# Optimization experiments

Hardware: AMD Instinct MI355X
Metric: run time of the kernel (lower is better)

The kernel has to match this reference:

```python
import jax, jax.numpy as jnp
import numpy as np

B, NPG, H, D = 16, 4096, 2, 64            # graphs, nodes/graph, heads, in_channels
N = B * NPG                                # 65536 total nodes
E_PER = 32768                              # edges per graph (avg degree 8)
E = B * E_PER                              # 524288 total edges
K_ORDER = 4
BETA = 0.5
D_OUT = 64


def setup_inputs():
    key = jax.random.key(0)
    k = jax.random.split(key, 10)
    x = jax.random.normal(k[0], (N, D), jnp.float32)
    # intra-graph random edges (block-diagonal adjacency)
    src = jax.random.randint(k[1], (B, E_PER), 0, NPG)
    dst = jax.random.randint(k[2], (B, E_PER), 0, NPG)
    off = (jnp.arange(B) * NPG)[:, None]
    edge_index = jnp.stack([(src + off).reshape(-1), (dst + off).reshape(-1)], axis=0)
    batch = jnp.arange(N) // NPG
    s = 1.0 / np.sqrt(D)
    Wq = jax.random.normal(k[3], (D, D * H), jnp.float32) * s
    bq = jnp.zeros((D * H,), jnp.float32)
    Wk = jax.random.normal(k[4], (D, D * H), jnp.float32) * s
    bk = jnp.zeros((D * H,), jnp.float32)
    Wo = jax.random.normal(k[5], (D * H, D_OUT), jnp.float32) * (1.0 / np.sqrt(D * H))
    bo = jnp.zeros((D_OUT,), jnp.float32)
    return {"x": x, "edge_index": edge_index, "batch": batch,
            "Wq": Wq, "bq": bq, "Wk": Wk, "bk": bk, "Wo": Wo, "bo": bo}


def reference(x, edge_index, batch, Wq, bq, Wk, bk, Wo, bo):
    Nn = x.shape[0]
    q = (x @ Wq + bq).reshape(Nn, H, D)
    k = (x @ Wk + bk).reshape(Nn, H, D)
    qs = q / jnp.linalg.norm(q, axis=2, keepdims=True)
    ks = k / jnp.linalg.norm(k, axis=2, keepdims=True)

    # symmetric-normalized transposed adjacency: adj_t[col_e, row_e] = w_e
    row, col = edge_index[0], edge_index[1]
    w = jnp.ones((row.shape[0],), x.dtype)
    deg = jax.ops.segment_sum(w, col, num_segments=N)
    dinv = jnp.where(deg > 0, deg ** -0.5, 0.0)
    val = dinv[col] * w * dinv[row]

    def gcn(xs):  # xs [N,H,D]; out[i] = sum_{e: col_e==i} val_e * xs[row_e]
        return jax.ops.segment_sum(val[:, None, None] * xs[row], col, num_segments=N)

    # ragged block <-> padded batch conversion (block-sorted batch ids)
    counts = jax.ops.segment_sum(jnp.ones((Nn,), jnp.int32), batch, num_segments=B)
    starts = jnp.concatenate([jnp.zeros((1,), jnp.int32), jnp.cumsum(counts)[:-1]])
    pos = jnp.arange(Nn) - starts[batch]

    def to_batch(v):
        return jnp.zeros((B, NPG) + v.shape[1:], v.dtype).at[batch, pos].set(v)

    def to_block(v):
        return v[batch, pos]

    qs_b, ks_b = to_batch(qs), to_batch(ks)      # [B, NPG, H, D]
    xs = jnp.broadcast_to(x[:, None, :], (Nn, H, D))
    xs_b = to_batch(xs)

    # linear (kernelized) attention; note source adds B (=qs.shape[0]) to the
    # denominator and uses the pre-loop xs_batch for every iteration -- kept faithful.
    kvs = jnp.einsum('blhm,blhd->bhmd', ks_b, xs_b)
    qkvs = jnp.einsum('bnhm,bhmd->bnhd', qs_b, kvs)
    num = qkvs + xs_b.sum(axis=1)[:, None]                       # [B,NPG,H,D]
    den = jnp.einsum('bnhm,bhm->bnh', qs_b, ks_b.sum(axis=1))[..., None] + float(B)
    attn_blk = to_block(num / den)                               # [N,H,D]

    for _ in range(K_ORDER):
        xs = xs + BETA * gcn(xs) + (1.0 - BETA) * attn_blk

    return (xs.reshape(Nn, H * D) @ Wo + bo) / H
```

## Files before the change

kernel.cpp:

```cpp
#include <hip/hip_runtime.h>

#define N_NODES 65536
#define B_G     16
#define NPG_    4096
#define H_H     2
#define D_D     64
#define HD      128
#define E_E     524288
#define D_OUT   64


__global__ void deg_kernel(const int* __restrict__ col, int* __restrict__ degi) {
    int e = blockIdx.x * 256 + threadIdx.x;
    if (e < E_E) atomicAdd(&degi[col[e]], 1);
}

__global__ void scan1(const int* __restrict__ degi, int* __restrict__ ptr,
                      int* __restrict__ bsums, float* __restrict__ dinv) {
    __shared__ int lds[256];
    int t = threadIdx.x;
    int i = blockIdx.x * 256 + t;
    int v = degi[i];
    dinv[i] = (v > 0) ? (1.0f / sqrtf((float)v)) : 0.0f;
    lds[t] = v;
    __syncthreads();
    for (int off = 1; off < 256; off <<= 1) {
        int tmp = (t >= off) ? lds[t - off] : 0;
        __syncthreads();
        lds[t] += tmp;
        __syncthreads();
    }
    ptr[i] = lds[t] - v;
    if (t == 255) bsums[blockIdx.x] = lds[255];
}

__global__ void scan3(int* __restrict__ ptr, const int* __restrict__ bsums) {
    __shared__ int red[256];
    int t = threadIdx.x;
    red[t] = (t < (int)blockIdx.x) ? bsums[t] : 0;
    __syncthreads();
    for (int off = 128; off > 0; off >>= 1) {
        if (t < off) red[t] += red[t + off];
        __syncthreads();
    }
    int i = blockIdx.x * 256 + t;
    ptr[i] += red[0];
    if (i == 0) ptr[N_NODES] = E_E;
}

__global__ void scatter_kernel(const int* __restrict__ row, const int* __restrict__ col,
                               const int* __restrict__ ptr, int* __restrict__ cursor,
                               const float* __restrict__ dinv,
                               int2* __restrict__ ep) {
    int e = blockIdx.x * 256 + threadIdx.x;
    if (e < E_E) {
        int c = col[e], r = row[e];
        int p = ptr[c] + atomicAdd(&cursor[c], 1);
        ep[p] = make_int2(r, __float_as_int(dinv[c] * dinv[r]));
    }
}

__global__ __launch_bounds__(256) void proj_kernel(
    const float* __restrict__ x,
    const float* __restrict__ Wq, const float* __restrict__ bq,
    const float* __restrict__ Wk, const float* __restrict__ bk,
    float* __restrict__ qs, float* __restrict__ ks) {
    __shared__ float4 wt4[16 * 64];
    __shared__ float4 xt4[128 * 16];
    int t = threadIdx.x;
    int qk = blockIdx.x & 1;
    int hh = (blockIdx.x >> 1) & 1;
    int nb = (blockIdx.x >> 2) * 128;
    const float* W = qk ? Wk : Wq;
    const float* bias = qk ? bk : bq;
    float* outp = qk ? ks : qs;

    for (int i = t; i < 1024; i += 256) {
        int k4 = i >> 6, c = i & 63;
        int cc = hh * 64 + c;
        wt4[i] = make_float4(W[(4 * k4 + 0) * 128 + cc], W[(4 * k4 + 1) * 128 + cc],
                             W[(4 * k4 + 2) * 128 + cc], W[(4 * k4 + 3) * 128 + cc]);
    }
    const float4* xg = (const float4*)(x + (size_t)nb * 64);
    for (int i = t; i < 2048; i += 256) {
        int node = i >> 4, k4 = i & 15;
        xt4[node * 16 + (k4 ^ (node & 7))] = xg[i];
    }
    __syncthreads();

    int cg = t & 15;
    int ns = t >> 4;
    int sw = ns & 7;

    float acc[8][4];
#pragma unroll
    for (int i = 0; i < 8; ++i)
#pragma unroll
        for (int j = 0; j < 4; ++j) acc[i][j] = 0.f;

    for (int k4 = 0; k4 < 16; ++k4) {
        float4 wv[4];
#pragma unroll
        for (int j = 0; j < 4; ++j) wv[j] = wt4[k4 * 64 + cg + 16 * j];
        int kx = k4 ^ sw;
#pragma unroll
        for (int i = 0; i < 8; ++i) {
            float4 xv = xt4[(ns + 16 * i) * 16 + kx];
#pragma unroll
            for (int j = 0; j < 4; ++j)
                acc[i][j] += wv[j].x * xv.x + wv[j].y * xv.y +
                             wv[j].z * xv.z + wv[j].w * xv.w;
        }
    }

    float bcol[4];
#pragma unroll
    for (int j = 0; j < 4; ++j) bcol[j] = bias[hh * 64 + cg + 16 * j];

#pragma unroll
    for (int i = 0; i < 8; ++i) {
#pragma unroll
        for (int j = 0; j < 4; ++j) acc[i][j] += bcol[j];
        float s = acc[i][0] * acc[i][0] + acc[i][1] * acc[i][1] +
                  acc[i][2] * acc[i][2] + acc[i][3] * acc[i][3];
#pragma unroll
        for (int off = 8; off > 0; off >>= 1) s += __shfl_xor(s, off);
        float r = rsqrtf(s);
        size_t base = (size_t)(nb + ns + 16 * i) * 128 + hh * 64 + cg;
#pragma unroll
        for (int j = 0; j < 4; ++j) outp[base + 16 * j] = acc[i][j] * r;
    }
}

__global__ __launch_bounds__(256) void kvs_part(
    const float* __restrict__ ks, const float* __restrict__ x,
    float* __restrict__ partials, float* __restrict__ ksum, float* __restrict__ xsum) {
    int bid = blockIdx.x;
    int chunk = bid & 31;
    int bh = bid >> 5;
    int b = bh >> 1, h = bh & 1;
    int t = threadIdx.x;
    int mrow = t >> 4, dcol = t & 15;
    int m0 = mrow * 4, d0 = dcol * 4;
    __shared__ float kl[32 * 64];
    __shared__ float xl[32 * 64];
    float acc[4][4] = {{0}};
    float ksacc[4] = {0, 0, 0, 0};
    float xsacc[4] = {0, 0, 0, 0};
    int node0 = b * NPG_ + chunk * 128;
    for (int s = 0; s < 4; ++s) {
        int nb = node0 + s * 32;
        for (int i = t; i < 512; i += 256) {
            int l = i >> 4, q = i & 15;
            ((float4*)kl)[i] = *(const float4*)(ks + (size_t)(nb + l) * 128 + h * 64 + q * 4);
        }
        const float4* xg = (const float4*)(x + (size_t)nb * 64);
        for (int i = t; i < 512; i += 256) ((float4*)xl)[i] = xg[i];
        __syncthreads();
        for (int l = 0; l < 32; ++l) {
            float4 kv = *(float4*)(kl + l * 64 + m0);
            float4 xv = *(float4*)(xl + l * 64 + d0);
            float kk[4] = {kv.x, kv.y, kv.z, kv.w};
            float xx[4] = {xv.x, xv.y, xv.z, xv.w};
#pragma unroll
            for (int i = 0; i < 4; ++i)
#pragma unroll
                for (int j = 0; j < 4; ++j) acc[i][j] += kk[i] * xx[j];
            if (dcol == 0) {
#pragma unroll
                for (int i = 0; i < 4; ++i) ksacc[i] += kk[i];
            }
            if (mrow == 0) {
#pragma unroll
                for (int j = 0; j < 4; ++j) xsacc[j] += xx[j];
            }
        }
        __syncthreads();
    }
    float* pout = partials + (size_t)bid * 4096;
#pragma unroll
    for (int i = 0; i < 4; ++i)
        *(float4*)(pout + (m0 + i) * 64 + d0) =
            make_float4(acc[i][0], acc[i][1], acc[i][2], acc[i][3]);
    if (dcol == 0) {
#pragma unroll
        for (int i = 0; i < 4; ++i) atomicAdd(&ksum[bh * 64 + m0 + i], ksacc[i]);
    }
    if (mrow == 0 && h == 0) {
#pragma unroll
        for (int j = 0; j < 4; ++j) atomicAdd(&xsum[b * 64 + d0 + j], xsacc[j]);
    }
}

__global__ __launch_bounds__(256) void kvs_reduce(
    const float* __restrict__ partials, float* __restrict__ kvs) {
    int i = blockIdx.x * 256 + threadIdx.x;
    int bh = i >> 12, elem = i & 4095;
    const float* p = partials + (size_t)bh * 32 * 4096 + elem;
    float s = 0.f;
#pragma unroll
    for (int c = 0; c < 32; ++c) s += p[c * 4096];
    kvs[i] = s;
}

__global__ __launch_bounds__(256) void mwo_kernel(
    const float* __restrict__ kvs, const float* __restrict__ Wo,
    const float* __restrict__ xsum, float* __restrict__ M, float* __restrict__ C) {
    __shared__ float kv_l[64 * 64];
    __shared__ float wo_l[64 * 64];
    __shared__ float xs_l[64];
    int bh = blockIdx.x;
    int b = bh >> 1, h = bh & 1;
    int t = threadIdx.x;
    const float4* kvg = (const float4*)(kvs + (size_t)bh * 4096);
    for (int i = t; i < 1024; i += 256) ((float4*)kv_l)[i] = kvg[i];
    for (int i = t; i < 1024; i += 256) {
        int d = i >> 4;
        ((float4*)wo_l)[i] = *(const float4*)(Wo + (size_t)(h * 64 + d) * 64 + (i & 15) * 4);
    }
    if (t < 64) xs_l[t] = xsum[b * 64 + t];
    __syncthreads();

    int ccol = t & 15, mrow = t >> 4;
    int m0 = mrow * 4, c0 = ccol * 4;
    float acc[4][4] = {{0.f}};
    float cacc[4] = {0.f, 0.f, 0.f, 0.f};
    for (int d = 0; d < 64; ++d) {
        float4 wv = *(const float4*)(wo_l + d * 64 + c0);
        float kvv[4];
#pragma unroll
        for (int i = 0; i < 4; ++i) kvv[i] = kv_l[(m0 + i) * 64 + d];
#pragma unroll
        for (int i = 0; i < 4; ++i) {
            acc[i][0] += kvv[i] * wv.x; acc[i][1] += kvv[i] * wv.y;
            acc[i][2] += kvv[i] * wv.z; acc[i][3] += kvv[i] * wv.w;
        }
        if (mrow == 0) {
            float xv = xs_l[d];
            cacc[0] += xv * wv.x; cacc[1] += xv * wv.y;
            cacc[2] += xv * wv.z; cacc[3] += xv * wv.w;
        }
    }
    float* mo = M + (size_t)bh * 4096;
#pragma unroll
    for (int i = 0; i < 4; ++i)
        *(float4*)(mo + (m0 + i) * 64 + c0) =
            make_float4(acc[i][0], acc[i][1], acc[i][2], acc[i][3]);
    if (mrow == 0)
        *(float4*)(C + bh * 64 + c0) = make_float4(cacc[0], cacc[1], cacc[2], cacc[3]);
}

__global__ __launch_bounds__(256) void fatt_kernel(
    const float* __restrict__ qs, const float* __restrict__ M,
    const float* __restrict__ C, const float* __restrict__ ksum,
    float* __restrict__ a) {
    __shared__ float4 wt4[16 * 64];
    __shared__ float4 xt4[64 * 16];
    __shared__ float4 ksv[16];
    __shared__ float csv[64];
    int nb = blockIdx.x * 64;
    int b = nb >> 12;
    int t = threadIdx.x;
    int cg = t & 15;
    int ns = t >> 4;
    int sw = ns & 3;
    int n_t = ns * 4;

    float acc[4][4] = {{0.f}};

    for (int h = 0; h < 2; ++h) {
        int bh = b * 2 + h;
        const float* mp = M + (size_t)bh * 4096;
        for (int i = t; i < 1024; i += 256) {
            int k4 = i >> 6, c = i & 63;
            wt4[i] = make_float4(mp[(4 * k4 + 0) * 64 + c], mp[(4 * k4 + 1) * 64 + c],
                                 mp[(4 * k4 + 2) * 64 + c], mp[(4 * k4 + 3) * 64 + c]);
        }
        for (int i = t; i < 1024; i += 256) {
            int node = i >> 4, k4 = i & 15;
            xt4[i] = *(const float4*)(qs + (size_t)(nb + node) * 128 + h * 64 + 4 * k4);
        }
        if (t < 16) ksv[t] = *(const float4*)(ksum + bh * 64 + 4 * t);
        if (t < 64) csv[t] = C[bh * 64 + t];
        __syncthreads();

        float pacc[4][4] = {{0.f}};
        float den[4] = {0.f, 0.f, 0.f, 0.f};
        for (int k4 = 0; k4 < 16; ++k4) {
            int kk = k4 ^ sw;
            float4 kv = ksv[kk];
            float4 wv[4];
#pragma unroll
            for (int j = 0; j < 4; ++j) wv[j] = wt4[kk * 64 + cg + 16 * j];
#pragma unroll
            for (int i = 0; i < 4; ++i) {
                float4 xv = xt4[(n_t + i) * 16 + kk];
                den[i] += kv.x * xv.x + kv.y * xv.y + kv.z * xv.z + kv.w * xv.w;
#pragma unroll
                for (int j = 0; j < 4; ++j)
                    pacc[i][j] += wv[j].x * xv.x + wv[j].y * xv.y +
                                  wv[j].z * xv.z + wv[j].w * xv.w;
            }
        }
        float cc[4];
#pragma unroll
        for (int j = 0; j < 4; ++j) cc[j] = csv[cg + 16 * j];
#pragma unroll
        for (int i = 0; i < 4; ++i) {
            float inv = 1.0f / (den[i] + 16.0f);
#pragma unroll
            for (int j = 0; j < 4; ++j) acc[i][j] += (pacc[i][j] + cc[j]) * inv;
        }
        __syncthreads();
    }

#pragma unroll
    for (int i = 0; i < 4; ++i)
#pragma unroll
        for (int j = 0; j < 4; ++j)
            a[(size_t)(nb + n_t + i) * 64 + cg + 16 * j] = acc[i][j];
}

__global__ __launch_bounds__(256) void y0_kernel(
    const float* __restrict__ x, const float* __restrict__ Wo,
    float* __restrict__ y0) {
    __shared__ float4 wt4[16 * 64];
    __shared__ float4 xt4[64 * 16];
    int t = threadIdx.x;
    int nb = blockIdx.x * 64;

    for (int i = t; i < 1024; i += 256) {
        int k4 = i >> 6, c = i & 63;
        wt4[i] = make_float4(
            Wo[(4 * k4 + 0) * 64 + c] + Wo[(4 * k4 + 64) * 64 + c],
            Wo[(4 * k4 + 1) * 64 + c] + Wo[(4 * k4 + 65) * 64 + c],
            Wo[(4 * k4 + 2) * 64 + c] + Wo[(4 * k4 + 66) * 64 + c],
            Wo[(4 * k4 + 3) * 64 + c] + Wo[(4 * k4 + 67) * 64 + c]);
    }
    const float4* xg = (const float4*)(x + (size_t)nb * 64);
    for (int i = t; i < 1024; i += 256) xt4[i] = xg[i];
    __syncthreads();

    int cg = t & 15;
    int ns = t >> 4;
    int s = ns & 3;
    int n_t = ns * 4;

    float acc[4][4] = {{0.f}};
#pragma unroll 4
    for (int k4 = 0; k4 < 16; ++k4) {
        int kk = k4 ^ s;
        float4 xv0 = xt4[(n_t + 0) * 16 + kk];
        float4 xv1 = xt4[(n_t + 1) * 16 + kk];
        float4 xv2 = xt4[(n_t + 2) * 16 + kk];
        float4 xv3 = xt4[(n_t + 3) * 16 + kk];
#pragma unroll
        for (int j = 0; j < 4; ++j) {
            float4 wv = wt4[kk * 64 + cg + 16 * j];
            acc[0][j] += wv.x * xv0.x + wv.y * xv0.y + wv.z * xv0.z + wv.w * xv0.w;
            acc[1][j] += wv.x * xv1.x + wv.y * xv1.y + wv.z * xv1.z + wv.w * xv1.w;
            acc[2][j] += wv.x * xv2.x + wv.y * xv2.y + wv.z * xv2.z + wv.w * xv2.w;
            acc[3][j] += wv.x * xv3.x + wv.y * xv3.y + wv.z * xv3.z + wv.w * xv3.w;
        }
    }
#pragma unroll
    for (int i = 0; i < 4; ++i)
#pragma unroll
        for (int j = 0; j < 4; ++j)
            y0[(size_t)(nb + n_t + i) * 64 + cg + 16 * j] = acc[i][j];
}

template <int LAST>
__global__ __launch_bounds__(256) void gcn64_kernel(
    const float* __restrict__ yin, const float* __restrict__ a,
    const int* __restrict__ ptr, const int2* __restrict__ ep,
    float* __restrict__ yout, const float* __restrict__ bo) {
    int bid = blockIdx.x;
    int lbid = (bid & 7) * (N_NODES / 16 / 8) + (bid >> 3);
    int t = threadIdx.x;
    int n = lbid * 16 + (t >> 4);
    int lg = t & 15;
    int c4 = lg * 4;
    int e0 = ptr[n], e1 = ptr[n + 1];
    int cnt = e1 - e0;
    float4 acc = make_float4(0.f, 0.f, 0.f, 0.f);

    int2 q[16];
#pragma unroll
    for (int i = 0; i < 16; ++i) {
        int ee = e0 + i;
        if (ee > e1 - 1) ee = e1 - 1;
        if (ee < 0) ee = 0;
        q[i] = ep[ee];
    }
#pragma unroll
    for (int i = 0; i < 16; ++i) {
        if (i < cnt) {
            float v = __int_as_float(q[i].y);
            float4 xv = *(const float4*)(yin + (size_t)q[i].x * 64 + c4);
            acc.x += v * xv.x; acc.y += v * xv.y;
            acc.z += v * xv.z; acc.w += v * xv.w;
        }
    }
    for (int e = e0 + 16; e < e1; ++e) {
        int2 qq = ep[e];
        float v = __int_as_float(qq.y);
        float4 xv = *(const float4*)(yin + (size_t)qq.x * 64 + c4);
        acc.x += v * xv.x; acc.y += v * xv.y;
        acc.z += v * xv.z; acc.w += v * xv.w;
    }

    size_t idx = (size_t)n * 64 + c4;
    float4 self = *(const float4*)(yin + idx);
    float4 at = *(const float4*)(a + idx);
    float4 o;
    o.x = self.x + 0.5f * acc.x + 0.5f * at.x;
    o.y = self.y + 0.5f * acc.y + 0.5f * at.y;
    o.z = self.z + 0.5f * acc.z + 0.5f * at.z;
    o.w = self.w + 0.5f * acc.w + 0.5f * at.w;
    if (LAST) {
        float4 bv = *(const float4*)(bo + c4);
        o.x = (o.x + bv.x) * 0.5f;
        o.y = (o.y + bv.y) * 0.5f;
        o.z = (o.z + bv.z) * 0.5f;
        o.w = (o.w + bv.w) * 0.5f;
    }
    *(float4*)(yout + idx) = o;
}


extern "C" void kernel_launch(void* const* d_in, const int* in_sizes, int n_in,
                              void* d_out, int out_size, void* d_ws, size_t ws_size,
                              hipStream_t stream) {
    const float* x  = (const float*)d_in[0];
    const int* ei   = (const int*)d_in[1];
    const float* Wq = (const float*)d_in[3];
    const float* bq = (const float*)d_in[4];
    const float* Wk = (const float*)d_in[5];
    const float* bk = (const float*)d_in[6];
    const float* Wo = (const float*)d_in[7];
    const float* bo = (const float*)d_in[8];
    float* out = (float*)d_out;

    const int* row = ei;
    const int* col = ei + E_E;

    float* bufA = (float*)d_ws;
    float* bufB = bufA + (size_t)N_NODES * HD;
    float* bufC = bufB + (size_t)N_NODES * HD;
    int2*  ep   = (int2*)(bufC + (size_t)N_NODES * HD);
    float* kvs  = (float*)(ep + E_E);
    float* M    = kvs + 131072;
    float* Cc   = M + 131072;
    float* ksum = Cc + 2048;
    float* xsum = ksum + 2048;
    float* dinv = xsum + 1024;
    int* degi   = (int*)(dinv + N_NODES);
    int* cursor = degi + N_NODES;
    int* ptr    = cursor + N_NODES;
    int* bsums  = ptr + N_NODES + 1;

    float* qs_      = bufC;
    float* ks_      = bufB;
    float* a_       = bufA;
    float* yA       = bufA + (size_t)N_NODES * 64;
    float* partials = yA;
    float* yB       = bufB;

    hipMemsetAsync(degi, 0, (size_t)N_NODES * 2 * 4, stream);
    hipMemsetAsync(ksum, 0, (size_t)(2048 + 1024) * 4, stream);

    deg_kernel<<<E_E / 256, 256, 0, stream>>>(col, degi);
    scan1<<<N_NODES / 256, 256, 0, stream>>>(degi, ptr, bsums, dinv);
    scan3<<<N_NODES / 256, 256, 0, stream>>>(ptr, bsums);
    scatter_kernel<<<E_E / 256, 256, 0, stream>>>(row, col, ptr, cursor, dinv, ep);

    proj_kernel<<<2048, 256, 0, stream>>>(x, Wq, bq, Wk, bk, qs_, ks_);

    kvs_part<<<1024, 256, 0, stream>>>(ks_, x, partials, ksum, xsum);
    kvs_reduce<<<512, 256, 0, stream>>>(partials, kvs);
    mwo_kernel<<<32, 256, 0, stream>>>(kvs, Wo, xsum, M, Cc);
    fatt_kernel<<<1024, 256, 0, stream>>>(qs_, M, Cc, ksum, a_);

    y0_kernel<<<1024, 256, 0, stream>>>(x, Wo, yA);

    gcn64_kernel<0><<<N_NODES / 16, 256, 0, stream>>>(yA, a_, ptr, ep, yB, bo);
    gcn64_kernel<0><<<N_NODES / 16, 256, 0, stream>>>(yB, a_, ptr, ep, yA, bo);
    gcn64_kernel<0><<<N_NODES / 16, 256, 0, stream>>>(yA, a_, ptr, ep, yB, bo);
    gcn64_kernel<1><<<N_NODES / 16, 256, 0, stream>>>(yB, a_, ptr, ep, out, bo);
}
```

Baseline: 336.3 us.

## Fuse q/k projections into KV-reduction and attention kernels, drop qs/ks buffers

Removes the standalone projection kernel. The K projection and normalization now run inside the KV partial-sum kernel, which uses 64-node chunks and produces twice as many partials. The Q projection runs inside the attention kernel per head. This avoids writing and re-reading two N×128 float intermediates in global memory. In exchange, each block reloads the Wq/Wk tiles, uses more shared memory, and adds a sync. The reduce kernel now sums 64 partials instead of 32.

```diff
diff --git a/kernel.cpp b/kernel.cpp
--- a/kernel.cpp
+++ b/kernel.cpp
@@ -60,133 +60,103 @@
     }
 }
 
-__global__ __launch_bounds__(256) void proj_kernel(
+__global__ __launch_bounds__(256) void kvskp_kernel(
     const float* __restrict__ x,
-    const float* __restrict__ Wq, const float* __restrict__ bq,
     const float* __restrict__ Wk, const float* __restrict__ bk,
-    float* __restrict__ qs, float* __restrict__ ks) {
+    float* __restrict__ partials, float* __restrict__ ksum, float* __restrict__ xsum) {
+    __shared__ float4 xt4[64 * 16];
     __shared__ float4 wt4[16 * 64];
-    __shared__ float4 xt4[128 * 16];
-    int t = threadIdx.x;
-    int qk = blockIdx.x & 1;
-    int hh = (blockIdx.x >> 1) & 1;
-    int nb = (blockIdx.x >> 2) * 128;
-    const float* W = qk ? Wk : Wq;
-    const float* bias = qk ? bk : bq;
-    float* outp = qk ? ks : qs;
-
+    __shared__ float4 kt4[64 * 16];
+    int bid = blockIdx.x;
+    int chunk = bid & 63;
+    int bh = bid >> 6;
+    int b = bh >> 1, h = bh & 1;
+    int node0 = b * NPG_ + chunk * 64;
+    int t = threadIdx.x;
+
+    const float4* xg = (const float4*)(x + (size_t)node0 * 64);
+    for (int i = t; i < 1024; i += 256) xt4[i] = xg[i];
     for (int i = t; i < 1024; i += 256) {
         int k4 = i >> 6, c = i & 63;
-        int cc = hh * 64 + c;
-        wt4[i] = make_float4(W[(4 * k4 + 0) * 128 + cc], W[(4 * k4 + 1) * 128 + cc],
-                             W[(4 * k4 + 2) * 128 + cc], W[(4 * k4 + 3) * 128 + cc]);
-    }
-    const float4* xg = (const float4*)(x + (size_t)nb * 64);
-    for (int i = t; i < 2048; i += 256) {
-        int node = i >> 4, k4 = i & 15;
-        xt4[node * 16 + (k4 ^ (node & 7))] = xg[i];
+        int cc = h * 64 + c;
+        wt4[i] = make_float4(Wk[(4 * k4 + 0) * 128 + cc], Wk[(4 * k4 + 1) * 128 + cc],
+                             Wk[(4 * k4 + 2) * 128 + cc], Wk[(4 * k4 + 3) * 128 + cc]);
     }
     __syncthreads();
 
     int cg = t & 15;
     int ns = t >> 4;
-    int sw = ns & 7;
-
-    float acc[8][4];
-#pragma unroll
-    for (int i = 0; i < 8; ++i)
-#pragma unroll
-        for (int j = 0; j < 4; ++j) acc[i][j] = 0.f;
-
-    for (int k4 = 0; k4 < 16; ++k4) {
-        float4 wv[4];
-#pragma unroll
-        for (int j = 0; j < 4; ++j) wv[j] = wt4[k4 * 64 + cg + 16 * j];
-        int kx = k4 ^ sw;
-#pragma unroll
-        for (int i = 0; i < 8; ++i) {
-            float4 xv = xt4[(ns + 16 * i) * 16 + kx];
+    int s = ns & 3;
+    int n_t = ns * 4;
+    float* ktf = (float*)kt4;
+
+    {
+        float acc[4][4] = {{0.f}};
+        for (int k4 = 0; k4 < 16; ++k4) {
+            int kk = k4 ^ s;
+            float4 wv[4];
+#pragma unroll
+            for (int j = 0; j < 4; ++j) wv[j] = wt4[kk * 64 + cg + 16 * j];
+#pragma unroll
+            for (int i = 0; i < 4; ++i) {
+                float4 xv = xt4[(n_t + i) * 16 + kk];
+#pragma unroll
+                for (int j = 0; j < 4; ++j)
+                    acc[i][j] += wv[j].x * xv.x + wv[j].y * xv.y +
+                                 wv[j].z * xv.z + wv[j].w * xv.w;
+            }
+        }
+        float bcol[4];
+#pragma unroll
+        for (int j = 0; j < 4; ++j) bcol[j] = bk[h * 64 + cg + 16 * j];
+#pragma unroll
+        for (int i = 0; i < 4; ++i) {
+#pragma unroll
+            for (int j = 0; j < 4; ++j) acc[i][j] += bcol[j];
+            float sq = acc[i][0] * acc[i][0] + acc[i][1] * acc[i][1] +
+                       acc[i][2] * acc[i][2] + acc[i][3] * acc[i][3];
+#pragma unroll
+            for (int off = 8; off > 0; off >>= 1) sq += __shfl_xor(sq, off);
+            float r = rsqrtf(sq);
 #pragma unroll
             for (int j = 0; j < 4; ++j)
-                acc[i][j] += wv[j].x * xv.x + wv[j].y * xv.y +
-                             wv[j].z * xv.z + wv[j].w * xv.w;
-        }
-    }
-
-    float bcol[4];
-#pragma unroll
-    for (int j = 0; j < 4; ++j) bcol[j] = bias[hh * 64 + cg + 16 * j];
-
-#pragma unroll
-    for (int i = 0; i < 8; ++i) {
-#pragma unroll
-        for (int j = 0; j < 4; ++j) acc[i][j] += bcol[j];
-        float s = acc[i][0] * acc[i][0] + acc[i][1] * acc[i][1] +
-                  acc[i][2] * acc[i][2] + acc[i][3] * acc[i][3];
-#pragma unroll
-        for (int off = 8; off > 0; off >>= 1) s += __shfl_xor(s, off);
-        float r = rsqrtf(s);
-        size_t base = (size_t)(nb + ns + 16 * i) * 128 + hh * 64 + cg;
-#pragma unroll
-        for (int j = 0; j < 4; ++j) outp[base + 16 * j] = acc[i][j] * r;
-    }
-}
-
-__global__ __launch_bounds__(256) void kvs_part(
-    const float* __restrict__ ks, const float* __restrict__ x,
-    float* __restrict__ partials, float* __restrict__ ksum, float* __restrict__ xsum) {
-    int bid = blockIdx.x;
-    int chunk = bid & 31;
-    int bh = bid >> 5;
-    int b = bh >> 1, h = bh & 1;
-    int t = threadIdx.x;
-    int mrow = t >> 4, dcol = t & 15;
-    int m0 = mrow * 4, d0 = dcol * 4;
-    __shared__ float kl[32 * 64];
-    __shared__ float xl[32 * 64];
-    float acc[4][4] = {{0}};
-    float ksacc[4] = {0, 0, 0, 0};
-    float xsacc[4] = {0, 0, 0, 0};
-    int node0 = b * NPG_ + chunk * 128;
-    for (int s = 0; s < 4; ++s) {
-        int nb = node0 + s * 32;
-        for (int i = t; i < 512; i += 256) {
-            int l = i >> 4, q = i & 15;
-            ((float4*)kl)[i] = *(const float4*)(ks + (size_t)(nb + l) * 128 + h * 64 + q * 4);
-        }
-        const float4* xg = (const float4*)(x + (size_t)nb * 64);
-        for (int i = t; i < 512; i += 256) ((float4*)xl)[i] = xg[i];
-        __syncthreads();
-        for (int l = 0; l < 32; ++l) {
-            float4 kv = *(float4*)(kl + l * 64 + m0);
-            float4 xv = *(float4*)(xl + l * 64 + d0);
-            float kk[4] = {kv.x, kv.y, kv.z, kv.w};
-            float xx[4] = {xv.x, xv.y, xv.z, xv.w};
-#pragma unroll
-            for (int i = 0; i < 4; ++i)
-#pragma unroll
-                for (int j = 0; j < 4; ++j) acc[i][j] += kk[i] * xx[j];
-            if (dcol == 0) {
-#pragma unroll
-                for (int i = 0; i < 4; ++i) ksacc[i] += kk[i];
-            }
-            if (mrow == 0) {
-#pragma unroll
-                for (int j = 0; j < 4; ++j) xsacc[j] += xx[j];
-            }
-        }
-        __syncthreads();
+                ktf[(n_t + i) * 64 + cg + 16 * j] = acc[i][j] * r;
+        }
+    }
+    __syncthreads();
+
+    int m0 = ns * 4, d0 = cg * 4;
+    float acc[4][4] = {{0.f}};
+    float ksacc[4] = {0.f, 0.f, 0.f, 0.f};
+    float xsacc[4] = {0.f, 0.f, 0.f, 0.f};
+    for (int l = 0; l < 64; ++l) {
+        float4 kv = *(const float4*)(ktf + l * 64 + m0);
+        float4 xv = xt4[l * 16 + cg];
+        float kk[4] = {kv.x, kv.y, kv.z, kv.w};
+        float xx[4] = {xv.x, xv.y, xv.z, xv.w};
+#pragma unroll
+        for (int i = 0; i < 4; ++i)
+#pragma unroll
+            for (int j = 0; j < 4; ++j) acc[i][j] += kk[i] * xx[j];
+        if (cg == 0) {
+#pragma unroll
+            for (int i = 0; i < 4; ++i) ksacc[i] += kk[i];
+        }
+        if (ns == 0) {
+#pragma unroll
+            for (int j = 0; j < 4; ++j) xsacc[j] += xx[j];
+        }
     }
     float* pout = partials + (size_t)bid * 4096;
 #pragma unroll
     for (int i = 0; i < 4; ++i)
         *(float4*)(pout + (m0 + i) * 64 + d0) =
             make_float4(acc[i][0], acc[i][1], acc[i][2], acc[i][3]);
-    if (dcol == 0) {
+    if (cg == 0) {
 #pragma unroll
         for (int i = 0; i < 4; ++i) atomicAdd(&ksum[bh * 64 + m0 + i], ksacc[i]);
     }
-    if (mrow == 0 && h == 0) {
+    if (ns == 0 && h == 0) {
 #pragma unroll
         for (int j = 0; j < 4; ++j) atomicAdd(&xsum[b * 64 + d0 + j], xsacc[j]);
     }
@@ -196,10 +166,10 @@
     const float* __restrict__ partials, float* __restrict__ kvs) {
     int i = blockIdx.x * 256 + threadIdx.x;
     int bh = i >> 12, elem = i & 4095;
-    const float* p = partials + (size_t)bh * 32 * 4096 + elem;
+    const float* p = partials + (size_t)bh * 64 * 4096 + elem;
     float s = 0.f;
 #pragma unroll
-    for (int c = 0; c < 32; ++c) s += p[c * 4096];
+    for (int c = 0; c < 64; ++c) s += p[c * 4096];
     kvs[i] = s;
 }
 
@@ -251,11 +221,13 @@
 }
 
 __global__ __launch_bounds__(256) void fatt_kernel(
-    const float* __restrict__ qs, const float* __restrict__ M,
-    const float* __restrict__ C, const float* __restrict__ ksum,
-    float* __restrict__ a) {
-    __shared__ float4 wt4[16 * 64];
+    const float* __restrict__ x,
+    const float* __restrict__ Wq, const float* __restrict__ bq,
+    const float* __restrict__ M, const float* __restrict__ C,
+    const float* __restrict__ ksum, float* __restrict__ a) {
     __shared__ float4 xt4[64 * 16];
+    __shared__ float4 wu4[16 * 64];
+    __shared__ float4 qt4[64 * 16];
     __shared__ float4 ksv[16];
     __shared__ float csv[64];
     int nb = blockIdx.x * 64;
@@ -265,20 +237,62 @@
     int ns = t >> 4;
     int sw = ns & 3;
     int n_t = ns * 4;
+    float* qtf = (float*)qt4;
+
+    const float4* xg = (const float4*)(x + (size_t)nb * 64);
+    for (int i = t; i < 1024; i += 256) xt4[i] = xg[i];
 
     float acc[4][4] = {{0.f}};
 
     for (int h = 0; h < 2; ++h) {
         int bh = b * 2 + h;
+        __syncthreads();
+        for (int i = t; i < 1024; i += 256) {
+            int k4 = i >> 6, c = i & 63;
+            int cc = h * 64 + c;
+            wu4[i] = make_float4(Wq[(4 * k4 + 0) * 128 + cc], Wq[(4 * k4 + 1) * 128 + cc],
+                                 Wq[(4 * k4 + 2) * 128 + cc], Wq[(4 * k4 + 3) * 128 + cc]);
+        }
+        __syncthreads();
+        {
+            float qa[4][4] = {{0.f}};
+            for (int k4 = 0; k4 < 16; ++k4) {
+                int kk = k4 ^ sw;
+                float4 wv[4];
+#pragma unroll
+                for (int j = 0; j < 4; ++j) wv[j] = wu4[kk * 64 + cg + 16 * j];
+#pragma unroll
+                for (int i = 0; i < 4; ++i) {
+                    float4 xv = xt4[(n_t + i) * 16 + kk];
+#pragma unroll
+                    for (int j = 0; j < 4; ++j)
+                        qa[i][j] += wv[j].x * xv.x + wv[j].y * xv.y +
+                                    wv[j].z * xv.z + wv[j].w * xv.w;
+                }
+            }
+            float bcol[4];
+#pragma unroll
+            for (int j = 0; j < 4; ++j) bcol[j] = bq[h * 64 + cg + 16 * j];
+#pragma unroll
+            for (int i = 0; i < 4; ++i) {
+#pragma unroll
+                for (int j = 0; j < 4; ++j) qa[i][j] += bcol[j];
+                float sq = qa[i][0] * qa[i][0] + qa[i][1] * qa[i][1] +
+                           qa[i][2] * qa[i][2] + qa[i][3] * qa[i][3];
+#pragma unroll
+                for (int off = 8; off > 0; off >>= 1) sq += __shfl_xor(sq, off);
+                float r = rsqrtf(sq);
+#pragma unroll
+                for (int j = 0; j < 4; ++j)
+                    qtf[(n_t + i) * 64 + cg + 16 * j] = qa[i][j] * r;
+            }
+        }
+        __syncthreads();
         const float* mp = M + (size_t)bh * 4096;
         for (int i = t; i < 1024; i += 256) {
             int k4 = i >> 6, c = i & 63;
-            wt4[i] = make_float4(mp[(4 * k4 + 0) * 64 + c], mp[(4 * k4 + 1) * 64 + c],
+            wu4[i] = make_float4(mp[(4 * k4 + 0) * 64 + c], mp[(4 * k4 + 1) * 64 + c],
                                  mp[(4 * k4 + 2) * 64 + c], mp[(4 * k4 + 3) * 64 + c]);
-        }
-        for (int i = t; i < 1024; i += 256) {
-            int node = i >> 4, k4 = i & 15;
-            xt4[i] = *(const float4*)(qs + (size_t)(nb + node) * 128 + h * 64 + 4 * k4);
         }
         if (t < 16) ksv[t] = *(const float4*)(ksum + bh * 64 + 4 * t);
         if (t < 64) csv[t] = C[bh * 64 + t];
@@ -291,10 +305,10 @@
             float4 kv = ksv[kk];
             float4 wv[4];
 #pragma unroll
-            for (int j = 0; j < 4; ++j) wv[j] = wt4[kk * 64 + cg + 16 * j];
+            for (int j = 0; j < 4; ++j) wv[j] = wu4[kk * 64 + cg + 16 * j];
 #pragma unroll
             for (int i = 0; i < 4; ++i) {
-                float4 xv = xt4[(n_t + i) * 16 + kk];
+                float4 xv = qt4[(n_t + i) * 16 + kk];
                 den[i] += kv.x * xv.x + kv.y * xv.y + kv.z * xv.z + kv.w * xv.w;
 #pragma unroll
                 for (int j = 0; j < 4; ++j)
@@ -311,7 +325,6 @@
 #pragma unroll
             for (int j = 0; j < 4; ++j) acc[i][j] += (pacc[i][j] + cc[j]) * inv;
         }
-        __syncthreads();
     }
 
 #pragma unroll
@@ -460,12 +473,10 @@
     int* ptr    = cursor + N_NODES;
     int* bsums  = ptr + N_NODES + 1;
 
-    float* qs_      = bufC;
-    float* ks_      = bufB;
     float* a_       = bufA;
     float* yA       = bufA + (size_t)N_NODES * 64;
-    float* partials = yA;
     float* yB       = bufB;
+    float* partials = bufC;
 
     hipMemsetAsync(degi, 0, (size_t)N_NODES * 2 * 4, stream);
     hipMemsetAsync(ksum, 0, (size_t)(2048 + 1024) * 4, stream);
@@ -475,12 +486,10 @@
     scan3<<<N_NODES / 256, 256, 0, stream>>>(ptr, bsums);
     scatter_kernel<<<E_E / 256, 256, 0, stream>>>(row, col, ptr, cursor, dinv, ep);
 
-    proj_kernel<<<2048, 256, 0, stream>>>(x, Wq, bq, Wk, bk, qs_, ks_);
-
-    kvs_part<<<1024, 256, 0, stream>>>(ks_, x, partials, ksum, xsum);
+    kvskp_kernel<<<2048, 256, 0, stream>>>(x, Wk, bk, partials, ksum, xsum);
     kvs_reduce<<<512, 256, 0, stream>>>(partials, kvs);
     mwo_kernel<<<32, 256, 0, stream>>>(kvs, Wo, xsum, M, Cc);
-    fatt_kernel<<<1024, 256, 0, stream>>>(qs_, M, Cc, ksum, a_);
+    fatt_kernel<<<1024, 256, 0, stream>>>(x, Wq, bq, M, Cc, ksum, a_);
 
     y0_kernel<<<1024, 256, 0, stream>>>(x, Wo, yA);
 
```

Result: slower. 353.1 us (+5.0%).
